# Performance work log

Measured on AMD Instinct MI355X. Metric: run time of the kernel, lower is better.

The kernel has to match this reference:

```python
import jax, jax.numpy as jnp
import numpy as np

LN_EPS = 1e-5

def _layernorm(x, g, b):
    mu = jnp.mean(x, axis=-1, keepdims=True)
    var = jnp.mean(jnp.square(x - mu), axis=-1, keepdims=True)
    return (x - mu) * jax.lax.rsqrt(var + LN_EPS) * g + b

def setup_inputs() -> dict:
    key = jax.random.key(0)
    ks = jax.random.split(key, 12)
    B, S, E = 8, 4096, 512
    H, DK = 64, 8          # d_k = E // H = 8 qubits per head
    NQ_FFN, FFN = 8, 2048
    TWO_PI = 2.0 * np.pi
    x = jax.random.normal(ks[0], (B, S, E), dtype=jnp.float32)
    # trainable RX phases per attention head/wire; trainable RY phases for FFN qubits
    theta_attn = jax.random.uniform(ks[1], (H, DK), dtype=jnp.float32, maxval=TWO_PI)
    theta_ffn = jax.random.uniform(ks[2], (NQ_FFN,), dtype=jnp.float32, maxval=TWO_PI)
    s_e = 1.0 / np.sqrt(E)
    W_comb = jax.random.uniform(ks[3], (E, E), dtype=jnp.float32, minval=-s_e, maxval=s_e)
    b_comb = jax.random.uniform(ks[4], (E,), dtype=jnp.float32, minval=-s_e, maxval=s_e)
    s_q = 1.0 / np.sqrt(NQ_FFN)
    W1 = jax.random.uniform(ks[5], (FFN, NQ_FFN), dtype=jnp.float32, minval=-s_q, maxval=s_q)
    b1 = jax.random.uniform(ks[6], (FFN,), dtype=jnp.float32, minval=-s_q, maxval=s_q)
    s_f = 1.0 / np.sqrt(FFN)
    W2 = jax.random.uniform(ks[7], (E, FFN), dtype=jnp.float32, minval=-s_f, maxval=s_f)
    b2 = jax.random.uniform(ks[8], (E,), dtype=jnp.float32, minval=-s_f, maxval=s_f)
    ln1_g = jnp.ones((E,), jnp.float32); ln1_b = jnp.zeros((E,), jnp.float32)
    ln2_g = jnp.ones((E,), jnp.float32); ln2_b = jnp.zeros((E,), jnp.float32)
    return {"x": x, "theta_attn": theta_attn, "W_comb": W_comb, "b_comb": b_comb,
            "ln1_g": ln1_g, "ln1_b": ln1_b, "theta_ffn": theta_ffn,
            "W1": W1, "b1": b1, "W2": W2, "b2": b2, "ln2_g": ln2_g, "ln2_b": ln2_b}

def reference(x, theta_attn, W_comb, b_comb, ln1_g, ln1_b, theta_ffn, W1, b1, W2, b2, ln2_g, ln2_b):
    B, S, E = x.shape
    H, DK = theta_attn.shape
    NQ = theta_ffn.shape[0]
    # Quantum attention heads: RX(x) then RX(theta) on |0> per wire -> <Z> = cos(x+theta)
    q = jnp.cos(x.reshape(B, S, H, DK) + theta_attn)  # [B,S,H,DK]
    attn_out = jnp.einsum('bse,fe->bsf', q.reshape(B, S, E), W_comb) + b_comb
    x1 = _layernorm(x + attn_out, ln1_g, ln1_b)
    # Quantum FFN layer: RY(x) then RY(theta) -> <Z> = cos(x+theta), first NQ features only
    fq = jnp.cos(x1[..., :NQ] + theta_ffn)            # [B,S,NQ]
    h = jax.nn.relu(jnp.einsum('bsq,fq->bsf', fq, W1) + b1)
    ffn_out = jnp.einsum('bsf,ef->bse', h, W2) + b2
    return _layernorm(x1 + ffn_out, ln2_g, ln2_b)
```

## Files before the change

### kernel.cpp

```cpp
#include <hip/hip_runtime.h>
#include <stdint.h>

typedef unsigned short u16;
typedef __bf16 bf16x8 __attribute__((ext_vector_type(8)));
typedef float f32x4 __attribute__((ext_vector_type(4)));

#define AS1(p) ((const __attribute__((address_space(1))) void*)(p))
#define AS3(p) ((__attribute__((address_space(3))) void*)(p))

__device__ __forceinline__ float b2f(u16 v){
    union { unsigned u; float f; } x; x.u = ((unsigned)v) << 16; return x.f;
}
__device__ __forceinline__ u16 f2b(float f){
    union { float f; unsigned u; } x; x.f = f;
    unsigned r = x.u + 0x7FFFu + ((x.u >> 16) & 1u);
    return (u16)(r >> 16);
}

__global__ __launch_bounds__(256) void probe_kernel(
    const u16* p0,const u16* p1,const u16* p2,const u16* p3,const u16* p4,
    const u16* p5,const u16* p6,const u16* p7,const u16* p8,const u16* p9,
    const u16* p10,const u16* p11,const u16* p12,
    int n0,int n1,int n2,int n3,int n4,int n5,int n6,int n7,int n8,int n9,
    int n10,int n11,int n12, int* flags)
{
    const u16* p; int n;
    switch (blockIdx.x) {
        case 0: p=p0; n=n0; break;   case 1: p=p1; n=n1; break;
        case 2: p=p2; n=n2; break;   case 3: p=p3; n=n3; break;
        case 4: p=p4; n=n4; break;   case 5: p=p5; n=n5; break;
        case 6: p=p6; n=n6; break;   case 7: p=p7; n=n7; break;
        case 8: p=p8; n=n8; break;   case 9: p=p9; n=n9; break;
        case 10: p=p10; n=n10; break; case 11: p=p11; n=n11; break;
        default: p=p12; n=n12; break;
    }
    int pairs = n >> 1; if (pairs > 2048) pairs = 2048;
    int strong = 0, znz = 0, tot = 0;
    for (int k = threadIdx.x; k < pairs; k += 256) {
        u16 lo = p[2*k], hi = p[2*k+1];
        int eh = (hi >> 7) & 0xFF;
        int el = (lo >> 7) & 0xFF;
        if (eh >= 0xF0 || (eh >= 1 && eh <= 0x40)) strong = 1;
        if (el >= 0xF0 || (el >= 1 && el <= 0x40)) strong = 1;
        if (lo == 0 && hi != 0) znz++;
        tot++;
    }
    __shared__ int ss, sz, st;
    if (threadIdx.x == 0) { ss = 0; sz = 0; st = 0; }
    __syncthreads();
    if (strong) atomicOr(&ss, 1);
    if (znz) atomicAdd(&sz, znz);
    atomicAdd(&st, tot);
    __syncthreads();
    if (threadIdx.x == 0) {
        flags[blockIdx.x] = (ss || (2 * sz > st)) ? 1 : 0;
        if (blockIdx.x == 0) flags[15] = 0;
    }
}

__global__ __launch_bounds__(256) void convert_kernel(
    const void* sWc, const void* sW2, const void* sW1,
    const void* sTa, const void* sBc, const void* sG1, const void* sB1l,
    const void* sTf, const void* sB1, const void* sB2, const void* sG2, const void* sB2l,
    u16* wbase, const int* flags)
{
    int b = blockIdx.x;
    const void* src; u16* dst; int n, fi, lb, tof32 = 0;
    if (b < 128)      { src=sWc; dst=wbase;          n=262144;  fi=2;  lb=b; }
    else if (b < 640) { src=sW2; dst=wbase+262144;   n=1048576; fi=9;  lb=b-128; }
    else if (b >= 643 && b < 651) { src=sW1; dst=wbase+1312256; n=16384; fi=7; lb=b-643; }
    else {
        lb = 0;
        switch (b) {
            case 640: src=sTa;  dst=wbase+1310720; n=512;  fi=1;  break;
            case 641: src=sBc;  dst=wbase+1311232; n=512;  fi=3;  break;
            case 642: src=sB2;  dst=wbase+1311744; n=512;  fi=10; break;
            case 651: src=sB1;  dst=wbase+1328640; n=2048; fi=8;  break;
            case 652: src=sG1;  dst=wbase+1330688; n=512;  fi=4;  break;
            case 653: src=sB1l; dst=wbase+1331200; n=512;  fi=5;  break;
            case 654: src=sG2;  dst=wbase+1331712; n=512;  fi=11; break;
            case 655: src=sB2l; dst=wbase+1332224; n=512;  fi=12; break;
            default:  src=sTf;  dst=wbase+1332736; n=8;    fi=6;  tof32=1; break;
        }
    }
    int i = lb * 256 + threadIdx.x;
    if (i * 8 >= n) return;
    if (tof32) {
        float* fd = (float*)dst;
        if (flags[fi]) {
            const float4* s = (const float4*)src;
            ((float4*)fd)[i*2] = s[i*2]; ((float4*)fd)[i*2+1] = s[i*2+1];
        } else {
            union { uint4 v; u16 h[8]; } sb;
            sb.v = ((const uint4*)src)[i];
            #pragma unroll
            for (int j = 0; j < 8; j++) fd[i*8+j] = b2f(sb.h[j]);
        }
        return;
    }
    if (flags[fi]) {
        const float4* s = (const float4*)src;
        float4 a = s[i*2], c = s[i*2+1];
        union { uint4 v; u16 h[8]; } o;
        o.h[0]=f2b(a.x); o.h[1]=f2b(a.y); o.h[2]=f2b(a.z); o.h[3]=f2b(a.w);
        o.h[4]=f2b(c.x); o.h[5]=f2b(c.y); o.h[6]=f2b(c.z); o.h[7]=f2b(c.w);
        ((uint4*)dst)[i] = o.v;
    } else {
        ((uint4*)dst)[i] = ((const uint4*)src)[i];
    }
}

__global__ __launch_bounds__(256) void qgen_kernel(
    const void* __restrict__ x, const u16* __restrict__ theta,
    u16* __restrict__ q, const int* flags)
{
    const int idx = blockIdx.x * 256 + threadIdx.x;
    const int col0 = (idx * 8) & 511;
    union { uint4 v; u16 h[8]; } tb;
    tb.v = *(const uint4*)(theta + col0);
    float xv[8];
    if (flags[0]) {
        const float4* p = (const float4*)x + idx * 2;
        float4 a = p[0], b = p[1];
        xv[0]=a.x; xv[1]=a.y; xv[2]=a.z; xv[3]=a.w;
        xv[4]=b.x; xv[5]=b.y; xv[6]=b.z; xv[7]=b.w;
    } else {
        union { uint4 v; u16 h[8]; } xb;
        xb.v = ((const uint4*)x)[idx];
        #pragma unroll
        for (int e = 0; e < 8; e++) xv[e] = b2f(xb.h[e]);
    }
    union { uint4 v; u16 h[8]; } o;
    #pragma unroll
    for (int e = 0; e < 8; e++) o.h[e] = f2b(__cosf(xv[e] + b2f(tb.h[e])));
    ((uint4*)q)[idx] = o.v;
}

__global__ __launch_bounds__(256, 3) void gemm1_fused(
    const u16* __restrict__ q, const void* __restrict__ x,
    const u16* __restrict__ Wt, const u16* __restrict__ bias,
    u16* __restrict__ dst, int mtiles, const int* flags)
{
    __shared__ __align__(16) u16 As[2][128 * 64];
    __shared__ __align__(16) u16 Bs[2][128 * 64];
    const int K = 512, N = 512;
    const int tid  = threadIdx.x;
    const int lane = tid & 63;
    const int w    = tid >> 6;

    const int blk = blockIdx.x;
    const int xcd = blk & 7;
    const int j   = blk >> 3;
    const int per = mtiles >> 3;
    const int mt  = xcd * per + (j >> 2);
    const int nt  = j & 3;
    const int m0 = mt * 128;
    const int n0 = nt * 128;

    const int srow = lane >> 3;
    const int scol = ((lane & 7) ^ srow) * 8;
    const int wm = (w >> 1) * 64;
    const int wn = (w & 1) * 64;
    const int fr   = lane & 15;
    const int quad = lane >> 4;
    const int fx   = fr & 7;
    const int isf32 = flags[0];

    f32x4 acc[4][4];
    #pragma unroll
    for (int i = 0; i < 4; i++)
        #pragma unroll
        for (int jj = 0; jj < 4; jj++)
            acc[i][jj] = f32x4{0.f, 0.f, 0.f, 0.f};

    const u16* Abase = q  + (size_t)m0 * K + scol;
    const u16* Bbase = Wt + (size_t)n0 * K + scol;

    #pragma unroll
    for (int i = 0; i < 4; i++) {
        int c = w * 4 + i;
        int row = c * 8 + srow;
        __builtin_amdgcn_global_load_lds(AS1(Abase + (size_t)row * K),
                                         AS3(&As[0][c * 512]), 16, 0, 0);
        __builtin_amdgcn_global_load_lds(AS1(Bbase + (size_t)row * K),
                                         AS3(&Bs[0][c * 512]), 16, 0, 0);
    }

    int cur = 0;
    for (int kt = 0; kt < K; kt += 64) {
        __syncthreads();
        if (kt + 64 < K) {
            int nxt = cur ^ 1;
            #pragma unroll
            for (int i = 0; i < 4; i++) {
                int c = w * 4 + i;
                int row = c * 8 + srow;
                __builtin_amdgcn_global_load_lds(
                    AS1(Abase + (size_t)row * K + kt + 64),
                    AS3(&As[nxt][c * 512]), 16, 0, 0);
                __builtin_amdgcn_global_load_lds(
                    AS1(Bbase + (size_t)row * K + kt + 64),
                    AS3(&Bs[nxt][c * 512]), 16, 0, 0);
            }
        }
        #pragma unroll
        for (int kk = 0; kk < 2; kk++) {
            bf16x8 af[4], bfr[4];
            #pragma unroll
            for (int mi = 0; mi < 4; mi++)
                af[mi] = *(const bf16x8*)(&As[cur][(wm + mi * 16 + fr) * 64 +
                                          (((kk * 4 + quad) ^ fx) * 8)]);
            #pragma unroll
            for (int ni = 0; ni < 4; ni++)
                bfr[ni] = *(const bf16x8*)(&Bs[cur][(wn + ni * 16 + fr) * 64 +
                                           (((kk * 4 + quad) ^ fx) * 8)]);
            #pragma unroll
            for (int mi = 0; mi < 4; mi++)
                #pragma unroll
                for (int ni = 0; ni < 4; ni++)
                    acc[mi][ni] = __builtin_amdgcn_mfma_f32_16x16x32_bf16(
                        af[mi], bfr[ni], acc[mi][ni], 0, 0, 0);
        }
        cur ^= 1;
    }

    #pragma unroll
    for (int mi = 0; mi < 4; mi++) {
        #pragma unroll
        for (int ni = 0; ni < 4; ni++) {
            int n = n0 + wn + ni * 16 + fr;
            float bn = b2f(bias[n]);
            #pragma unroll
            for (int r = 0; r < 4; r++) {
                int m = m0 + wm + mi * 16 + quad * 4 + r;
                float rv = isf32 ? ((const float*)x)[(size_t)m * N + n]
                                 : b2f(((const u16*)x)[(size_t)m * N + n]);
                dst[(size_t)m * N + n] = f2b(acc[mi][ni][r] + bn + rv);
            }
        }
    }
}

__global__ __launch_bounds__(256) void gemm2_fused(
    const u16* __restrict__ fq, const u16* __restrict__ W1, const u16* __restrict__ b1,
    const u16* __restrict__ Wt, const u16* __restrict__ bias,
    const u16* __restrict__ res, u16* __restrict__ dst, int mtiles)
{
    __shared__ __align__(16) u16 As[128 * 64];
    __shared__ __align__(16) u16 Bs[2][128 * 64];
    const int K = 2048, N = 512;
    const int tid  = threadIdx.x;
    const int lane = tid & 63;
    const int w    = tid >> 6;

    const int blk = blockIdx.x;
    const int xcd = blk & 7;
    const int j   = blk >> 3;
    const int per = mtiles >> 3;
    const int mt  = xcd * per + (j >> 2);
    const int nt  = j & 3;
    const int m0 = mt * 128;
    const int n0 = nt * 128;

    const int srow = lane >> 3;
    const int scol = ((lane & 7) ^ srow) * 8;
    const int wm = (w >> 1) * 64;
    const int wn = (w & 1) * 64;
    const int fr   = lane & 15;
    const int quad = lane >> 4;
    const int fx   = fr & 7;

    bf16x8 fqf[8];
    #pragma unroll
    for (int t2 = 0; t2 < 8; t2++) {
        union { uint4 v; bf16x8 b; } z; z.v = uint4{0,0,0,0};
        if (quad == 0) z.v = *(const uint4*)(fq + (size_t)(m0 + t2 * 16 + fr) * 8);
        fqf[t2] = z.b;
    }
    union { uint4 v; bf16x8 b; } w1u; w1u.v = uint4{0,0,0,0};
    if (quad == 0) w1u.v = *(const uint4*)(W1 + (size_t)(w * 16 + fr) * 8);
    uint2 b1v = *(const uint2*)(b1 + w * 16 + quad * 4);

    f32x4 acc[4][4];
    #pragma unroll
    for (int i = 0; i < 4; i++)
        #pragma unroll
        for (int jj = 0; jj < 4; jj++)
            acc[i][jj] = f32x4{0.f, 0.f, 0.f, 0.f};

    const u16* Bbase = Wt + (size_t)n0 * K + scol;
    #pragma unroll
    for (int i = 0; i < 4; i++) {
        int c = w * 4 + i;
        int row = c * 8 + srow;
        __builtin_amdgcn_global_load_lds(AS1(Bbase + (size_t)row * K),
                                         AS3(&Bs[0][c * 512]), 16, 0, 0);
    }

    int cur = 0;
    for (int kt = 0; kt < K; kt += 64) {
        __syncthreads();
        {
            const u16* pb = (const u16*)&b1v;
            f32x4 binit = {b2f(pb[0]), b2f(pb[1]), b2f(pb[2]), b2f(pb[3])};
            const int g   = w * 2 + (quad >> 1);
            const int off = (quad & 1) * 4;
            #pragma unroll
            for (int t2 = 0; t2 < 8; t2++) {
                f32x4 hv = __builtin_amdgcn_mfma_f32_16x16x32_bf16(
                    w1u.b, fqf[t2], binit, 0, 0, 0);
                union { uint2 u; __bf16 h[4]; } hw;
                hw.h[0] = (__bf16)fmaxf(hv[0], 0.f);
                hw.h[1] = (__bf16)fmaxf(hv[1], 0.f);
                hw.h[2] = (__bf16)fmaxf(hv[2], 0.f);
                hw.h[3] = (__bf16)fmaxf(hv[3], 0.f);
                int m = t2 * 16 + fr;
                *(uint2*)(As + m * 64 + ((g ^ (m & 7)) * 8 + off)) = hw.u;
            }
        }
        __syncthreads();
        if (kt + 64 < K) {
            if (quad == 0)
                w1u.v = *(const uint4*)(W1 + (size_t)(kt + 64 + w * 16 + fr) * 8);
            b1v = *(const uint2*)(b1 + kt + 64 + w * 16 + quad * 4);
            int nxt = cur ^ 1;
            #pragma unroll
            for (int i = 0; i < 4; i++) {
                int c = w * 4 + i;
                int row = c * 8 + srow;
                __builtin_amdgcn_global_load_lds(
                    AS1(Bbase + (size_t)row * K + kt + 64),
                    AS3(&Bs[nxt][c * 512]), 16, 0, 0);
            }
        }
        #pragma unroll
        for (int kk = 0; kk < 2; kk++) {
            bf16x8 af[4], bfr[4];
            #pragma unroll
            for (int mi = 0; mi < 4; mi++)
                af[mi] = *(const bf16x8*)(As + (wm + mi * 16 + fr) * 64 +
                                          (((kk * 4 + quad) ^ fx) * 8));
            #pragma unroll
            for (int ni = 0; ni < 4; ni++)
                bfr[ni] = *(const bf16x8*)(&Bs[cur][(wn + ni * 16 + fr) * 64 +
                                           (((kk * 4 + quad) ^ fx) * 8)]);
            #pragma unroll
            for (int mi = 0; mi < 4; mi++)
                #pragma unroll
                for (int ni = 0; ni < 4; ni++)
                    acc[mi][ni] = __builtin_amdgcn_mfma_f32_16x16x32_bf16(
                        af[mi], bfr[ni], acc[mi][ni], 0, 0, 0);
        }
        cur ^= 1;
    }

    #pragma unroll
    for (int mi = 0; mi < 4; mi++) {
        #pragma unroll
        for (int ni = 0; ni < 4; ni++) {
            int n = n0 + wn + ni * 16 + fr;
            float bn = b2f(bias[n]);
            #pragma unroll
            for (int r = 0; r < 4; r++) {
                int m = m0 + wm + mi * 16 + quad * 4 + r;
                float rv = b2f(res[(size_t)m * N + n]);
                dst[(size_t)m * N + n] = f2b(acc[mi][ni][r] + bn + rv);
            }
        }
    }
}

__global__ __launch_bounds__(512) void ln1_kernel(
    const u16* __restrict__ y1, const u16* __restrict__ g, const u16* __restrict__ b,
    const float* __restrict__ tf, u16* __restrict__ x1, u16* __restrict__ fqout)
{
    __shared__ __align__(16) float xs8[64][8];
    const int t = threadIdx.x;
    const int wv = t >> 6, l = t & 63;
    const size_t rbase = (size_t)blockIdx.x * 64;

    union { uint4 v; u16 s[8]; } gb, bb;
    gb.v = *(const uint4*)(g + l * 8);
    bb.v = *(const uint4*)(b + l * 8);

    #pragma unroll
    for (int i = 0; i < 8; i++) {
        int lr = wv * 8 + i;
        union { uint4 v; u16 s[8]; } yb;
        yb.v = ((const uint4*)(y1 + (rbase + lr) * 512))[l];
        float xv[8], s = 0.f, ss = 0.f;
        #pragma unroll
        for (int jj = 0; jj < 8; jj++) {
            xv[jj] = b2f(yb.s[jj]); s += xv[jj]; ss += xv[jj] * xv[jj];
        }
        #pragma unroll
        for (int o = 32; o > 0; o >>= 1) { s += __shfl_down(s, o); ss += __shfl_down(ss, o); }
        s = __shfl(s, 0); ss = __shfl(ss, 0);
        float mu = s * (1.f / 512.f);
        float rs = rsqrtf(ss * (1.f / 512.f) - mu * mu + 1e-5f);
        union { uint4 v; u16 s[8]; } ob;
        float xn[8];
        #pragma unroll
        for (int jj = 0; jj < 8; jj++) {
            xn[jj] = (xv[jj] - mu) * rs * b2f(gb.s[jj]) + b2f(bb.s[jj]);
            ob.s[jj] = f2b(xn[jj]);
        }
        ((uint4*)(x1 + (rbase + lr) * 512))[l] = ob.v;
        if (l == 0) {
            #pragma unroll
            for (int jj = 0; jj < 8; jj++) xs8[lr][jj] = xn[jj];
        }
    }
    __syncthreads();
    {
        int r = t >> 3, jj = t & 7;
        fqout[(rbase + r) * 8 + jj] = f2b(__cosf(xs8[r][jj] + tf[jj]));
    }
}

__global__ __launch_bounds__(256) void ln2_kernel(
    const u16* __restrict__ z, const u16* __restrict__ g, const u16* __restrict__ b,
    void* __restrict__ out, const int* flags)
{
    const int t = threadIdx.x;
    const int wv = t >> 6, l = t & 63;
    const size_t row = (size_t)blockIdx.x * 4 + wv;

    union { uint4 v; u16 s[8]; } zb, gb, bb;
    zb.v = ((const uint4*)(z + row * 512))[l];
    gb.v = *(const uint4*)(g + l * 8);
    bb.v = *(const uint4*)(b + l * 8);
    float xv[8], s = 0.f, ss = 0.f;
    #pragma unroll
    for (int jj = 0; jj < 8; jj++) { xv[jj] = b2f(zb.s[jj]); s += xv[jj]; ss += xv[jj]*xv[jj]; }
    #pragma unroll
    for (int o = 32; o > 0; o >>= 1) { s += __shfl_down(s, o); ss += __shfl_down(ss, o); }
    s = __shfl(s, 0); ss = __shfl(ss, 0);
    float mu = s * (1.f / 512.f);
    float rs = rsqrtf(ss * (1.f / 512.f) - mu * mu + 1e-5f);
    float xn[8];
    #pragma unroll
    for (int jj = 0; jj < 8; jj++)
        xn[jj] = (xv[jj] - mu) * rs * b2f(gb.s[jj]) + b2f(bb.s[jj]);
    if (flags[0]) {
        float* po = (float*)out + row * 512 + l * 8;
        float4 o0{xn[0],xn[1],xn[2],xn[3]}, o1{xn[4],xn[5],xn[6],xn[7]};
        *(float4*)po = o0; *(float4*)(po + 4) = o1;
    } else {
        union { uint4 v; u16 s[8]; } ob;
        #pragma unroll
        for (int jj = 0; jj < 8; jj++) ob.s[jj] = f2b(xn[jj]);
        ((uint4*)((u16*)out + row * 512))[l] = ob.v;
    }
}

extern "C" void kernel_launch(void* const* d_in, const int* in_sizes, int n_in,
                              void* d_out, int out_size, void* d_ws, size_t ws_size,
                              hipStream_t stream)
{
    u16* ws16 = (u16*)d_ws;
    u16* W     = ws16;
    int* flags = (int*)(ws16 + 1332752);
    u16* fq  = ws16 + 1332800;
    u16* x1  = ws16 + 1594944;
    u16* q   = x1;
    u16* y1  = ws16 + 18372160;
    u16* z   = y1;

    const u16*  wWc  = W;
    const u16*  wW2  = W + 262144;
    const u16*  wTa  = W + 1310720;
    const u16*  wBc  = W + 1311232;
    const u16*  wB2  = W + 1311744;
    const u16*  wW1  = W + 1312256;
    const u16*  wB1  = W + 1328640;
    const u16*  wG1  = W + 1330688;
    const u16*  wB1l = W + 1331200;
    const u16*  wG2  = W + 1331712;
    const u16*  wB2l = W + 1332224;
    const float* wTf = (const float*)(W + 1332736);

    probe_kernel<<<13, 256, 0, stream>>>(
        (const u16*)d_in[0], (const u16*)d_in[1], (const u16*)d_in[2],
        (const u16*)d_in[3], (const u16*)d_in[4], (const u16*)d_in[5],
        (const u16*)d_in[6], (const u16*)d_in[7], (const u16*)d_in[8],
        (const u16*)d_in[9], (const u16*)d_in[10], (const u16*)d_in[11],
        (const u16*)d_in[12],
        in_sizes[0], in_sizes[1], in_sizes[2], in_sizes[3], in_sizes[4],
        in_sizes[5], in_sizes[6], in_sizes[7], in_sizes[8], in_sizes[9],
        in_sizes[10], in_sizes[11], in_sizes[12], flags);

    convert_kernel<<<657, 256, 0, stream>>>(
        d_in[2], d_in[9], d_in[7], d_in[1], d_in[3], d_in[4], d_in[5],
        d_in[6], d_in[8], d_in[10], d_in[11], d_in[12], (u16*)W, flags);

    qgen_kernel<<<8192, 256, 0, stream>>>(d_in[0], wTa, q, flags);

    gemm1_fused<<<1024, 256, 0, stream>>>(
        q, d_in[0], wWc, wBc, y1, 256, flags);

    ln1_kernel<<<512, 512, 0, stream>>>(y1, wG1, wB1l, wTf, x1, fq);

    gemm2_fused<<<1024, 256, 0, stream>>>(
        fq, wW1, wB1, wW2, wB2, x1, z, 256);

    ln2_kernel<<<8192, 256, 0, stream>>>(z, wG2, wB2l, d_out, flags);
}
```

Measured before the change: 325.6 us.

## Compute FFN hidden activations in registers, dropping LDS staging and a barrier

```diff
diff --git a/kernel.cpp b/kernel.cpp
--- a/kernel.cpp
+++ b/kernel.cpp
@@ -241,12 +241,11 @@
     }
 }
 
-__global__ __launch_bounds__(256) void gemm2_fused(
+__global__ __launch_bounds__(256, 3) void gemm2_fused(
     const u16* __restrict__ fq, const u16* __restrict__ W1, const u16* __restrict__ b1,
     const u16* __restrict__ Wt, const u16* __restrict__ bias,
     const u16* __restrict__ res, u16* __restrict__ dst, int mtiles)
 {
-    __shared__ __align__(16) u16 As[128 * 64];
     __shared__ __align__(16) u16 Bs[2][128 * 64];
     const int K = 2048, N = 512;
     const int tid  = threadIdx.x;
@@ -270,16 +269,25 @@
     const int quad = lane >> 4;
     const int fx   = fr & 7;
 
-    bf16x8 fqf[8];
-    #pragma unroll
-    for (int t2 = 0; t2 < 8; t2++) {
+    bf16x8 fqf[4];
+    #pragma unroll
+    for (int mi = 0; mi < 4; mi++) {
         union { uint4 v; bf16x8 b; } z; z.v = uint4{0,0,0,0};
-        if (quad == 0) z.v = *(const uint4*)(fq + (size_t)(m0 + t2 * 16 + fr) * 8);
-        fqf[t2] = z.b;
-    }
-    union { uint4 v; bf16x8 b; } w1u; w1u.v = uint4{0,0,0,0};
-    if (quad == 0) w1u.v = *(const uint4*)(W1 + (size_t)(w * 16 + fr) * 8);
-    uint2 b1v = *(const uint2*)(b1 + w * 16 + quad * 4);
+        if (quad == 0) z.v = *(const uint4*)(fq + (size_t)(m0 + wm + mi * 16 + fr) * 8);
+        fqf[mi] = z.b;
+    }
+
+    const int krow = ((fr >> 2) * 8) + (fr & 3);
+
+    union { uint4 v; bf16x8 b; } w1f[4];
+    uint2 b1f[4];
+    #pragma unroll
+    for (int g = 0; g < 4; g++) {
+        w1f[g].v = uint4{0,0,0,0};
+        if (quad == 0)
+            w1f[g].v = *(const uint4*)(W1 + (size_t)((g >> 1) * 32 + (g & 1) * 4 + krow) * 8);
+        b1f[g] = *(const uint2*)(b1 + (g >> 1) * 32 + (g & 1) * 4 + quad * 8);
+    }
 
     f32x4 acc[4][4];
     #pragma unroll
@@ -300,29 +308,7 @@
     int cur = 0;
     for (int kt = 0; kt < K; kt += 64) {
         __syncthreads();
-        {
-            const u16* pb = (const u16*)&b1v;
-            f32x4 binit = {b2f(pb[0]), b2f(pb[1]), b2f(pb[2]), b2f(pb[3])};
-            const int g   = w * 2 + (quad >> 1);
-            const int off = (quad & 1) * 4;
-            #pragma unroll
-            for (int t2 = 0; t2 < 8; t2++) {
-                f32x4 hv = __builtin_amdgcn_mfma_f32_16x16x32_bf16(
-                    w1u.b, fqf[t2], binit, 0, 0, 0);
-                union { uint2 u; __bf16 h[4]; } hw;
-                hw.h[0] = (__bf16)fmaxf(hv[0], 0.f);
-                hw.h[1] = (__bf16)fmaxf(hv[1], 0.f);
-                hw.h[2] = (__bf16)fmaxf(hv[2], 0.f);
-                hw.h[3] = (__bf16)fmaxf(hv[3], 0.f);
-                int m = t2 * 16 + fr;
-                *(uint2*)(As + m * 64 + ((g ^ (m & 7)) * 8 + off)) = hw.u;
-            }
-        }
-        __syncthreads();
         if (kt + 64 < K) {
-            if (quad == 0)
-                w1u.v = *(const uint4*)(W1 + (size_t)(kt + 64 + w * 16 + fr) * 8);
-            b1v = *(const uint2*)(b1 + kt + 64 + w * 16 + quad * 4);
             int nxt = cur ^ 1;
             #pragma unroll
             for (int i = 0; i < 4; i++) {
@@ -335,21 +321,41 @@
         }
         #pragma unroll
         for (int kk = 0; kk < 2; kk++) {
-            bf16x8 af[4], bfr[4];
-            #pragma unroll
-            for (int mi = 0; mi < 4; mi++)
-                af[mi] = *(const bf16x8*)(As + (wm + mi * 16 + fr) * 64 +
-                                          (((kk * 4 + quad) ^ fx) * 8));
+            bf16x8 bfr[4];
             #pragma unroll
             for (int ni = 0; ni < 4; ni++)
                 bfr[ni] = *(const bf16x8*)(&Bs[cur][(wn + ni * 16 + fr) * 64 +
                                            (((kk * 4 + quad) ^ fx) * 8)]);
-            #pragma unroll
-            for (int mi = 0; mi < 4; mi++)
+            const u16* pb0 = (const u16*)&b1f[kk * 2 + 0];
+            const u16* pb1 = (const u16*)&b1f[kk * 2 + 1];
+            f32x4 c0 = {b2f(pb0[0]), b2f(pb0[1]), b2f(pb0[2]), b2f(pb0[3])};
+            f32x4 c1 = {b2f(pb1[0]), b2f(pb1[1]), b2f(pb1[2]), b2f(pb1[3])};
+            #pragma unroll
+            for (int mi = 0; mi < 4; mi++) {
+                f32x4 hv0 = __builtin_amdgcn_mfma_f32_16x16x32_bf16(
+                    w1f[kk * 2 + 0].b, fqf[mi], c0, 0, 0, 0);
+                f32x4 hv1 = __builtin_amdgcn_mfma_f32_16x16x32_bf16(
+                    w1f[kk * 2 + 1].b, fqf[mi], c1, 0, 0, 0);
+                bf16x8 af;
+                #pragma unroll
+                for (int r = 0; r < 4; r++) {
+                    af[r]     = (__bf16)fmaxf(hv0[r], 0.f);
+                    af[4 + r] = (__bf16)fmaxf(hv1[r], 0.f);
+                }
                 #pragma unroll
                 for (int ni = 0; ni < 4; ni++)
                     acc[mi][ni] = __builtin_amdgcn_mfma_f32_16x16x32_bf16(
-                        af[mi], bfr[ni], acc[mi][ni], 0, 0, 0);
+                        af, bfr[ni], acc[mi][ni], 0, 0, 0);
+            }
+        }
+        if (kt + 64 < K) {
+            #pragma unroll
+            for (int g = 0; g < 4; g++) {
+                if (quad == 0)
+                    w1f[g].v = *(const uint4*)(W1 +
+                        (size_t)(kt + 64 + (g >> 1) * 32 + (g & 1) * 4 + krow) * 8);
+                b1f[g] = *(const uint2*)(b1 + kt + 64 + (g >> 1) * 32 + (g & 1) * 4 + quad * 8);
+            }
         }
         cur ^= 1;
     }
```

New measurement: 336.3 us. +3.3%, slower.
